# Kernel tuning notes

Measured on AMD Instinct MI355X. Metric: run time of the kernel, lower is better.

Reference implementation:

```python
import jax, jax.numpy as jnp
import numpy as np

B, C, H, W = 32, 64, 64, 64
K, D = 512, 64  # num_embeddings, embedding_dim (C == D)


def setup_inputs() -> dict:
    key = jax.random.key(0)
    k1, k2 = jax.random.split(key)
    z_e = jax.random.normal(k1, (B, C, H, W), dtype=jnp.float32)
    # torch init: uniform_(-1/K, 1/K)
    codebook = jax.random.uniform(k2, (K, D), dtype=jnp.float32,
                                  minval=-1.0 / K, maxval=1.0 / K)
    return {"z_e": z_e, "codebook": codebook}


def reference(z_e, codebook):
    # [B,C,H,W] -> [B,H,W,C] -> [N,C]
    z_flat = jnp.transpose(z_e, (0, 2, 3, 1)).reshape(-1, z_e.shape[1])
    distances = (jnp.sum(z_flat ** 2, axis=1, keepdims=True)
                 + jnp.sum(codebook ** 2, axis=1)
                 - 2.0 * jnp.matmul(z_flat, codebook.T))
    encoding_indices = jnp.argmin(distances, axis=1)  # [N]
    z_q_flat = codebook[encoding_indices]             # [N,D]
    # NOTE: original torch code does z_q_flat.view(z_e.shape) WITHOUT
    # inverse permute; replicate that raw reinterpretation exactly.
    z_q = z_q_flat.reshape(z_e.shape)
    return z_q, encoding_indices
```

## Files before the change

kernel.cpp:

```cpp
#include <hip/hip_runtime.h>


typedef __attribute__((ext_vector_type(4))) float fl4;

__global__ __launch_bounds__(256)
void vq9(const float* __restrict__ z,
         const float* __restrict__ cb,
         float* __restrict__ out)
{
    __shared__ float s2l[512];
    __shared__ int   ifin[256];

    const int tid = threadIdx.x;
    const int n0  = blockIdx.x << 8;
    const int n   = n0 + tid;

    for (int k = tid; k < 512; k += 256) {
        const float* row = cb + k * 64;
        float p[8];
        #pragma unroll
        for (int j = 0; j < 8; ++j) p[j] = __fmul_rn(row[j], row[j]);
        #pragma unroll
        for (int m = 1; m < 8; ++m)
            #pragma unroll
            for (int j = 0; j < 8; ++j)
                p[j] = __fadd_rn(p[j], __fmul_rn(row[m * 8 + j], row[m * 8 + j]));
        s2l[k] = __fadd_rn(__fadd_rn(__fadd_rn(p[0], p[1]), __fadd_rn(p[2], p[3])),
                           __fadd_rn(__fadd_rn(p[4], p[5]), __fadd_rn(p[6], p[7])));
    }
    __syncthreads();

    const size_t base = (size_t)(n >> 12) * 262144 + (size_t)(n & 4095);
    float zv[64];
    float p[8];
    #pragma unroll
    for (int c = 0; c < 64; ++c) {
        const float v = z[base + (size_t)c * 4096];
        zv[c] = v;
        const float sq = __fmul_rn(v, v);
        if (c < 8) p[c] = sq;
        else       p[c & 7] = __fadd_rn(p[c & 7], sq);
    }
    const float s1 = __fadd_rn(__fadd_rn(__fadd_rn(p[0], p[1]), __fadd_rn(p[2], p[3])),
                               __fadd_rn(__fadd_rn(p[4], p[5]), __fadd_rn(p[6], p[7])));

    float best = 3.4e38f;
    int   bi   = 0;
    for (int k = 0; k < 512; ++k) {
        const float* row = cb + (size_t)k * 64;
        float m32 = 0.0f;
        #pragma unroll
        for (int c = 0; c < 64; ++c)
            m32 = fmaf(row[c], zv[c], m32);
        const float T = __fadd_rn(s1, s2l[k]);
        const float d = __fsub_rn(T, 2.0f * m32);
        if (d < best) { best = d; bi = k; }
    }
    ifin[tid] = bi;
    out[8388608 + n] = (float)bi;
    __syncthreads();

    float* ob = out + (size_t)n0 * 64;
    #pragma unroll
    for (int it = 0; it < 16; ++it) {
        const int o    = it * 1024 + tid * 4;
        const int sloc = o >> 6;
        const int c0   = o & 63;
        const int idx  = ifin[sloc] & 511;
        const fl4 v = *(const fl4*)(cb + idx * 64 + c0);
        *(fl4*)(ob + o) = v;
    }
}

extern "C" void kernel_launch(void* const* d_in, const int* in_sizes, int n_in,
                              void* d_out, int out_size, void* d_ws, size_t ws_size,
                              hipStream_t stream) {
    const float* z  = (const float*)d_in[0];
    const float* cb = (const float*)d_in[1];
    float* out = (float*)d_out;
    vq9<<<512, 256, 0, stream>>>(z, cb, out);
}
```

Baseline: 261.7 us.

## Split VQ into transpose kernel and codebook-per-thread distance kernel with wave argmin

The first kernel transposes z into point-major rows and writes per-point squared norms, using the output buffer as scratch. The second kernel maps one codebook row to each thread, held in registers. It loops over 128 points per block with uniform loads of the transposed z, and reduces the argmin across lanes with shuffles, a ballot and a cross-wave shared-memory merge. The aim is to move the work so codebook data stays in registers and the points are broadcast, instead of each thread scanning all 512 codebook rows. In exchange it adds an extra launch, a round trip of z through global memory, and a per-point shuffle reduction.

```diff
diff --git a/kernel.cpp b/kernel.cpp
--- a/kernel.cpp
+++ b/kernel.cpp
@@ -4,70 +4,126 @@
 typedef __attribute__((ext_vector_type(4))) float fl4;
 
 __global__ __launch_bounds__(256)
-void vq9(const float* __restrict__ z,
-         const float* __restrict__ cb,
-         float* __restrict__ out)
+void vq13a(const float* __restrict__ z, float* __restrict__ ow)
 {
-    __shared__ float s2l[512];
-    __shared__ int   ifin[256];
-
+    __shared__ float zl[256][65];
     const int tid = threadIdx.x;
     const int n0  = blockIdx.x << 8;
     const int n   = n0 + tid;
+    const size_t base = (size_t)(n >> 12) * 262144 + (size_t)(n & 4095);
 
-    for (int k = tid; k < 512; k += 256) {
-        const float* row = cb + k * 64;
-        float p[8];
-        #pragma unroll
-        for (int j = 0; j < 8; ++j) p[j] = __fmul_rn(row[j], row[j]);
-        #pragma unroll
-        for (int m = 1; m < 8; ++m)
-            #pragma unroll
-            for (int j = 0; j < 8; ++j)
-                p[j] = __fadd_rn(p[j], __fmul_rn(row[m * 8 + j], row[m * 8 + j]));
-        s2l[k] = __fadd_rn(__fadd_rn(__fadd_rn(p[0], p[1]), __fadd_rn(p[2], p[3])),
-                           __fadd_rn(__fadd_rn(p[4], p[5]), __fadd_rn(p[6], p[7])));
-    }
-    __syncthreads();
-
-    const size_t base = (size_t)(n >> 12) * 262144 + (size_t)(n & 4095);
-    float zv[64];
     float p[8];
     #pragma unroll
     for (int c = 0; c < 64; ++c) {
         const float v = z[base + (size_t)c * 4096];
-        zv[c] = v;
+        zl[tid][c] = v;
         const float sq = __fmul_rn(v, v);
         if (c < 8) p[c] = sq;
         else       p[c & 7] = __fadd_rn(p[c & 7], sq);
     }
-    const float s1 = __fadd_rn(__fadd_rn(__fadd_rn(p[0], p[1]), __fadd_rn(p[2], p[3])),
-                               __fadd_rn(__fadd_rn(p[4], p[5]), __fadd_rn(p[6], p[7])));
+    const float s1 = __fadd_rn(__fadd_rn(__fadd_rn(p[0],p[1]),__fadd_rn(p[2],p[3])),
+                               __fadd_rn(__fadd_rn(p[4],p[5]),__fadd_rn(p[6],p[7])));
+    ow[8388608 + n] = s1;
+    __syncthreads();
 
-    float best = 3.4e38f;
-    int   bi   = 0;
-    for (int k = 0; k < 512; ++k) {
-        const float* row = cb + (size_t)k * 64;
-        float m32 = 0.0f;
+    float* zt = ow + (size_t)n0 * 64;
+    #pragma unroll
+    for (int j = 0; j < 16; ++j) {
+        const int f  = j * 256 + tid;
+        const int nl = f >> 4, c0 = (f & 15) << 2;
+        fl4 v;
+        #pragma unroll
+        for (int e = 0; e < 4; ++e) v[e] = zl[nl][c0 + e];
+        *(fl4*)(zt + ((size_t)f << 2)) = v;
+    }
+}
+
+#define CBE(i) cbv[(i) >> 2][(i) & 3]
+
+__global__ __launch_bounds__(512, 4)
+void vq13b(const float* __restrict__ cb,
+           const float* __restrict__ zt,
+           const float* __restrict__ s1g,
+           float* __restrict__ ow)
+{
+    __shared__ float s1l[128];
+    __shared__ float cdl[8][128];
+    __shared__ int   ckl[8][128];
+    __shared__ int   ifin[128];
+
+    const int tid  = threadIdx.x;
+    const int w    = tid >> 6;
+    const int lane = tid & 63;
+    const int n0   = blockIdx.x << 7;
+    const int k    = (w << 6) + lane;
+
+    fl4 cbv[16];
+    {
+        const fl4* rp = (const fl4*)(cb + ((size_t)k << 6));
+        #pragma unroll
+        for (int j = 0; j < 16; ++j) cbv[j] = rp[j];
+    }
+    float s2k;
+    {
+        float q[8];
+        #pragma unroll
+        for (int j = 0; j < 8; ++j) q[j] = __fmul_rn(CBE(j), CBE(j));
+        #pragma unroll
+        for (int m = 1; m < 8; ++m)
+            #pragma unroll
+            for (int j = 0; j < 8; ++j) {
+                const float v = CBE(m * 8 + j);
+                q[j] = __fadd_rn(q[j], __fmul_rn(v, v));
+            }
+        s2k = __fadd_rn(__fadd_rn(__fadd_rn(q[0],q[1]),__fadd_rn(q[2],q[3])),
+                        __fadd_rn(__fadd_rn(q[4],q[5]),__fadd_rn(q[6],q[7])));
+    }
+
+    if (tid < 128) s1l[tid] = s1g[n0 + tid];
+    __syncthreads();
+
+    for (int s = 0; s < 128; ++s) {
+        const float* zr = zt + ((size_t)(n0 + s) << 6);
+        float m = 0.0f;
         #pragma unroll
         for (int c = 0; c < 64; ++c)
-            m32 = fmaf(row[c], zv[c], m32);
-        const float T = __fadd_rn(s1, s2l[k]);
-        const float d = __fsub_rn(T, 2.0f * m32);
-        if (d < best) { best = d; bi = k; }
+            m = fmaf(zr[c], CBE(c), m);
+        const float T = __fadd_rn(s1l[s], s2k);
+        const float d = __fsub_rn(T, 2.0f * m);
+
+        float dm = d;
+        #pragma unroll
+        for (int off = 1; off < 64; off <<= 1)
+            dm = fminf(dm, __shfl_xor(dm, off, 64));
+        const unsigned long long eq = __ballot(d == dm);
+        if (lane == 0) {
+            cdl[w][s] = dm;
+            ckl[w][s] = (w << 6) + (__ffsll((long long)eq) - 1);
+        }
     }
-    ifin[tid] = bi;
-    out[8388608 + n] = (float)bi;
     __syncthreads();
 
-    float* ob = out + (size_t)n0 * 64;
+    if (tid < 128) {
+        float bd = cdl[0][tid]; int bk = ckl[0][tid];
+        #pragma unroll
+        for (int ww = 1; ww < 8; ++ww) {
+            const float dw = cdl[ww][tid];
+            const int   kw = ckl[ww][tid];
+            if (dw < bd) { bd = dw; bk = kw; }
+        }
+        ifin[tid] = bk;
+        ow[8388608 + n0 + tid] = (float)bk;
+    }
+    __syncthreads();
+
+    float* ob = ow + ((size_t)n0 << 6);
     #pragma unroll
-    for (int it = 0; it < 16; ++it) {
-        const int o    = it * 1024 + tid * 4;
+    for (int it = 0; it < 4; ++it) {
+        const int o    = it * 2048 + (tid << 2);
         const int sloc = o >> 6;
         const int c0   = o & 63;
         const int idx  = ifin[sloc] & 511;
-        const fl4 v = *(const fl4*)(cb + idx * 64 + c0);
+        const fl4 v = *(const fl4*)(cb + ((size_t)idx << 6) + c0);
         *(fl4*)(ob + o) = v;
     }
 }
@@ -78,5 +134,6 @@
     const float* z  = (const float*)d_in[0];
     const float* cb = (const float*)d_in[1];
     float* out = (float*)d_out;
-    vq9<<<512, 256, 0, stream>>>(z, cb, out);
+    vq13a<<<512, 256, 0, stream>>>(z, out);
+    vq13b<<<1024, 512, 0, stream>>>(cb, out, out + 8388608, out);
 }
```

Result: no change. 264.4 us (+1.0%).
